# Optimization experiments

Measured on AMD Instinct MI355X. Metric: run time of the kernel, lower is better.

## Reference

```python
import jax, jax.numpy as jnp
import numpy as np

B_SZ, L, D_MODEL = 4, 4096, 512
D_INNER, N_HEADS, HEAD_DIM = 1024, 16, 64
D_STATE, D_CONV, CHUNK = 64, 4, 64
EPS = 1e-5


def setup_inputs() -> dict:
    key = jax.random.key(0)
    ks = jax.random.split(key, 12)
    return {
        'x': jax.random.normal(ks[0], (B_SZ, L, D_MODEL), jnp.float32),
        'W_in': jax.random.normal(ks[1], (D_MODEL, 2 * D_INNER), jnp.float32) * 0.02,
        'conv_x_kernel': jax.random.normal(ks[2], (D_CONV, 1, D_INNER), jnp.float32) * 0.1,
        'conv_x_bias': jnp.zeros((D_INNER,), jnp.float32),
        'conv_z_kernel': jax.random.normal(ks[3], (D_CONV, 1, D_INNER), jnp.float32) * 0.1,
        'conv_z_bias': jnp.zeros((D_INNER,), jnp.float32),
        'W_xdbl': jax.random.normal(ks[4], (D_INNER, N_HEADS + 2 * D_STATE), jnp.float32) * 0.02,
        'dt_bias': jax.random.normal(ks[5], (N_HEADS,), jnp.float32) * 0.5,
        'A_log': jax.random.uniform(ks[6], (N_HEADS,), jnp.float32, 0.0, 1.0),
        'D': jnp.ones((N_HEADS,), jnp.float32),
        'norm_weight': jnp.ones((D_INNER,), jnp.float32),
        'W_out': jax.random.normal(ks[7], (D_INNER, D_MODEL), jnp.float32) * 0.02,
    }


def dwconv(x, kernel, bias):
    # x: (b, l, d); kernel: (k, 1, d) depthwise, flax 'SAME' padding
    out = jax.lax.conv_general_dilated(
        x, kernel, window_strides=(1,), padding='SAME',
        dimension_numbers=('NWC', 'WIO', 'NWC'),
        feature_group_count=x.shape[-1])
    return out + bias


def segsum(a):
    # stable segment-sum: out[..., d, e] = sum_{e < i <= d} a[..., i]; -inf above diag
    T = a.shape[-1]
    a_rep = jnp.broadcast_to(a[..., :, None], a.shape + (T,))
    strict = jnp.tril(jnp.ones((T, T), bool), -1)
    seg = jnp.cumsum(jnp.where(strict, a_rep, 0.0), axis=-2)
    return jnp.where(jnp.tril(jnp.ones((T, T), bool)), seg, -jnp.inf)


def ssd(x, A, B, C, chunk):
    # x: (b,l,h,p), A: (b,l,h), B/C: (b,l,n) (single group, broadcast over heads)
    b, l, h, p = x.shape
    c = l // chunk
    x = x.reshape(b, c, chunk, h, p)
    A = A.reshape(b, c, chunk, h).transpose(0, 3, 1, 2)  # (b,h,c,l)
    B = B.reshape(b, c, chunk, -1)
    C = C.reshape(b, c, chunk, -1)
    A_cum = jnp.cumsum(A, axis=-1)
    Lmat = jnp.exp(segsum(A))  # (b,h,c,l,l)
    Y_diag = jnp.einsum('bcln,bcsn,bhcls,bcshp->bclhp', C, B, Lmat, x)
    decay_states = jnp.exp(A_cum[..., -1:] - A_cum)
    states = jnp.einsum('bcln,bhcl,bclhp->bchpn', B, decay_states, x)
    states = jnp.concatenate([jnp.zeros_like(states[:, :1]), states], axis=1)
    A_last = jnp.pad(A_cum[..., -1], ((0, 0), (0, 0), (1, 0)))
    decay_chunk = jnp.exp(segsum(A_last))  # (b,h,c+1,c+1)
    new_states = jnp.einsum('bhzc,bchpn->bzhpn', decay_chunk, states)
    states, final_state = new_states[:, :-1], new_states[:, -1]
    Y_off = jnp.einsum('bcln,bchpn,bhcl->bclhp', C, states, jnp.exp(A_cum))
    Y = (Y_diag + Y_off).reshape(b, l, h, p)
    return Y, final_state


def reference(x, W_in, conv_x_kernel, conv_x_bias, conv_z_kernel, conv_z_bias,
              W_xdbl, dt_bias, A_log, D, norm_weight, W_out):
    b, l, _ = x.shape
    xz = x @ W_in
    xi, z = jnp.split(xz, 2, axis=-1)
    xi = jax.nn.silu(dwconv(xi, conv_x_kernel, conv_x_bias))
    z = jax.nn.silu(dwconv(z, conv_z_kernel, conv_z_bias))
    x_dbl = xi @ W_xdbl  # (b,l,h+2n)
    dt = x_dbl[..., :N_HEADS]
    Bmat = x_dbl[..., N_HEADS:N_HEADS + D_STATE]
    Cmat = x_dbl[..., N_HEADS + D_STATE:]
    dt = jax.nn.softplus(dt + dt_bias)  # (b,l,h)
    A = -jnp.exp(A_log)  # (h,)
    xh = xi.reshape(b, l, N_HEADS, HEAD_DIM)
    y, _ = ssd(xh * dt[..., None], A * dt, Bmat, Cmat, CHUNK)
    y = y + xh * D[..., None]
    y = y.reshape(b, l, D_INNER)
    # gated RMSNorm (Mamba2 style): gate with silu(z), then rmsnorm with weight
    y = y * jax.nn.silu(z)
    y = y * jax.lax.rsqrt(jnp.mean(y * y, axis=-1, keepdims=True) + EPS) * norm_weight
    return y @ W_out
```

## Files before the change

### kernel.cpp

```cpp
#include <hip/hip_runtime.h>
#include <hip/hip_bf16.h>
#include <cstdint>

#define B_SZn 4
#define SEQ_L 4096
#define D_MODELn 512
#define D_INNERn 1024
#define N_HEADSn 16
#define HEAD_DIMn 64
#define D_STATEn 64
#define CHUNKn 64
#define NCHUNK (SEQ_L / CHUNKn)
#define BL (B_SZn * SEQ_L)
#define XDBL_N (N_HEADSn + 2 * D_STATEn)

typedef __hip_bfloat16 bf16;
typedef __bf16 bf16x8 __attribute__((ext_vector_type(8)));
typedef float f32x4 __attribute__((ext_vector_type(4)));

__device__ __forceinline__ float silu_f(float v) {
    return v / (1.0f + expf(-v));
}
__device__ __forceinline__ float b2f(unsigned short u) {
    return __uint_as_float((unsigned)u << 16);
}
__device__ __forceinline__ unsigned short f2b(float f) {
    bf16 h = __float2bfloat16(f);
    return *(unsigned short*)&h;
}
__device__ __forceinline__ void stf(float* p, float v) { *p = v; }
__device__ __forceinline__ void stf(bf16* p, float v) { *p = __float2bfloat16(v); }

__device__ __forceinline__ float4 us4_to_f4(ushort4 u) {
    float4 f;
    f.x = b2f(u.x); f.y = b2f(u.y); f.z = b2f(u.z); f.w = b2f(u.w);
    return f;
}

__device__ __forceinline__ void async_copy16(void* lds, const void* g) {
    __builtin_amdgcn_global_load_lds(
        (const __attribute__((address_space(1))) unsigned int*)g,
        (__attribute__((address_space(3))) unsigned int*)lds, 16, 0, 0);
}

__global__ __launch_bounds__(256) void cvt_f32_bf16(
    const float* __restrict__ in, bf16* __restrict__ out) {
    const int idx = blockIdx.x * 256 + threadIdx.x;
    float4 v = *(const float4*)(in + (size_t)idx * 4);
    ushort4 o;
    o.x = f2b(v.x); o.y = f2b(v.y); o.z = f2b(v.z); o.w = f2b(v.w);
    *(ushort4*)((unsigned short*)out + (size_t)idx * 4) = o;
}

__global__ __launch_bounds__(256) void transpose_cvt(
    const float* __restrict__ in, bf16* __restrict__ out, int R, int C) {
    __shared__ float t[32][33];
    const int bc = blockIdx.x * 32, br = blockIdx.y * 32;
    const int tx = threadIdx.x & 31, ty = threadIdx.x >> 5;
#pragma unroll
    for (int i = ty; i < 32; i += 8) {
        int r = br + i, c = bc + tx;
        t[i][tx] = (r < R && c < C) ? in[(size_t)r * C + c] : 0.f;
    }
    __syncthreads();
#pragma unroll
    for (int i = ty; i < 32; i += 8) {
        int c = bc + i, r = br + tx;
        if (c < C && r < R) out[(size_t)c * R + r] = __float2bfloat16(t[tx][i]);
    }
}

template <typename TO>
__global__ __launch_bounds__(256) void gemm_mfma(
    const bf16* __restrict__ A, const bf16* __restrict__ Bt,
    TO* __restrict__ C, int M, int N, int K) {
    __shared__ __align__(16) unsigned short Al[2][128 * 32];
    __shared__ __align__(16) unsigned short Bl[2][128 * 32];
    const int tid = threadIdx.x;
    const int wave = tid >> 6, lane = tid & 63;
    const int wm = (wave >> 1) * 64, wn = (wave & 1) * 64;
    int lin = blockIdx.y * gridDim.x + blockIdx.x;
    const int nwg = gridDim.x * gridDim.y;
    if ((nwg & 7) == 0) lin = (lin & 7) * (nwg >> 3) + (lin >> 3);
    const int bm = (lin / gridDim.x) * 128, bn = (lin % gridDim.x) * 128;
    f32x4 acc[4][4];
#pragma unroll
    for (int m = 0; m < 4; ++m)
#pragma unroll
        for (int n = 0; n < 4; ++n) acc[m][n] = (f32x4)(0.f);

    const int lrow = lane & 15, lk8 = (lane >> 4) * 8;
    const int srow = tid >> 2, sc8 = (tid & 3) * 8;
    for (int k0 = 0; k0 < K; k0 += 64) {
#pragma unroll
        for (int h = 0; h < 2; ++h) {
            const int kh = k0 + h * 32;
            async_copy16((char*)&Al[h][0] + (size_t)(wave * 64) * 16,
                         A + (size_t)(bm + srow) * K + kh + sc8);
            async_copy16((char*)&Al[h][0] + (size_t)(256 + wave * 64) * 16,
                         A + (size_t)(bm + 64 + srow) * K + kh + sc8);
            async_copy16((char*)&Bl[h][0] + (size_t)(wave * 64) * 16,
                         Bt + (size_t)(bn + srow) * K + kh + sc8);
            async_copy16((char*)&Bl[h][0] + (size_t)(256 + wave * 64) * 16,
                         Bt + (size_t)(bn + 64 + srow) * K + kh + sc8);
        }
        __syncthreads();
#pragma unroll
        for (int h = 0; h < 2; ++h) {
            bf16x8 af[4], bfr[4];
#pragma unroll
            for (int m = 0; m < 4; ++m)
                af[m] = *(const bf16x8*)(&Al[h][(wm + m * 16 + lrow) * 32 + lk8]);
#pragma unroll
            for (int n = 0; n < 4; ++n)
                bfr[n] = *(const bf16x8*)(&Bl[h][(wn + n * 16 + lrow) * 32 + lk8]);
#pragma unroll
            for (int m = 0; m < 4; ++m)
#pragma unroll
                for (int n = 0; n < 4; ++n)
                    acc[m][n] = __builtin_amdgcn_mfma_f32_16x16x32_bf16(
                        af[m], bfr[n], acc[m][n], 0, 0, 0);
        }
        __syncthreads();
    }
#pragma unroll
    for (int m = 0; m < 4; ++m) {
#pragma unroll
        for (int n = 0; n < 4; ++n) {
#pragma unroll
            for (int r = 0; r < 4; ++r) {
                int row = bm + wm + m * 16 + (lane >> 4) * 4 + r;
                int col = bn + wn + n * 16 + (lane & 15);
                if (row < M && col < N)
                    stf(&C[(size_t)row * N + col], acc[m][n][r]);
            }
        }
    }
}

template <typename TO>
__global__ __launch_bounds__(512) void gemm_mfma_wide(
    const bf16* __restrict__ A, const bf16* __restrict__ Bt,
    TO* __restrict__ C, int M, int N, int K) {
    __shared__ __align__(16) unsigned short Al[2][128 * 32];
    __shared__ __align__(16) unsigned short Bl[2][256 * 32];
    const int tid = threadIdx.x;
    const int wave = tid >> 6, lane = tid & 63;
    const int wm = (wave >> 2) * 64, wn = (wave & 3) * 64;
    int lin = blockIdx.y * gridDim.x + blockIdx.x;
    const int nwg = gridDim.x * gridDim.y;
    if ((nwg & 7) == 0) lin = (lin & 7) * (nwg >> 3) + (lin >> 3);
    const int bm = (lin / gridDim.x) * 128, bn = (lin % gridDim.x) * 256;
    f32x4 acc[4][4];
#pragma unroll
    for (int m = 0; m < 4; ++m)
#pragma unroll
        for (int n = 0; n < 4; ++n) acc[m][n] = (f32x4)(0.f);

    const int lrow = lane & 15, lk8 = (lane >> 4) * 8;
    const int srow = tid >> 2, sc8 = (tid & 3) * 8;
    for (int k0 = 0; k0 < K; k0 += 64) {
#pragma unroll
        for (int h = 0; h < 2; ++h) {
            const int kh = k0 + h * 32;
            async_copy16((char*)&Al[h][0] + (size_t)(wave * 64) * 16,
                         A + (size_t)(bm + srow) * K + kh + sc8);
            async_copy16((char*)&Bl[h][0] + (size_t)(wave * 64) * 16,
                         Bt + (size_t)(bn + srow) * K + kh + sc8);
            async_copy16((char*)&Bl[h][0] + (size_t)(512 + wave * 64) * 16,
                         Bt + (size_t)(bn + 128 + srow) * K + kh + sc8);
        }
        __syncthreads();
#pragma unroll
        for (int h = 0; h < 2; ++h) {
            bf16x8 af[4], bfr[4];
#pragma unroll
            for (int m = 0; m < 4; ++m)
                af[m] = *(const bf16x8*)(&Al[h][(wm + m * 16 + lrow) * 32 + lk8]);
#pragma unroll
            for (int n = 0; n < 4; ++n)
                bfr[n] = *(const bf16x8*)(&Bl[h][(wn + n * 16 + lrow) * 32 + lk8]);
#pragma unroll
            for (int m = 0; m < 4; ++m)
#pragma unroll
                for (int n = 0; n < 4; ++n)
                    acc[m][n] = __builtin_amdgcn_mfma_f32_16x16x32_bf16(
                        af[m], bfr[n], acc[m][n], 0, 0, 0);
        }
        __syncthreads();
    }
#pragma unroll
    for (int m = 0; m < 4; ++m) {
#pragma unroll
        for (int n = 0; n < 4; ++n) {
#pragma unroll
            for (int r = 0; r < 4; ++r) {
                int row = bm + wm + m * 16 + (lane >> 4) * 4 + r;
                int col = bn + wn + n * 16 + (lane & 15);
                if (row < M && col < N)
                    stf(&C[(size_t)row * N + col], acc[m][n][r]);
            }
        }
    }
}

__global__ __launch_bounds__(256) void conv_silu_kernel(
    const bf16* __restrict__ xz,
    const float* __restrict__ kx, const float* __restrict__ bx,
    const float* __restrict__ kz, const float* __restrict__ bz,
    bf16* __restrict__ xi, bf16* __restrict__ zo) {
    const int tid = threadIdx.x;
    const int d4 = tid * 4;
    const int blk = blockIdx.x;
    const int l0 = (blk * 8) & (SEQ_L - 1);
    const int b = (blk * 8) >> 12;
    const unsigned short* base = (const unsigned short*)xz +
                                 ((size_t)b * SEQ_L) * (2 * D_INNERn);
    float4 wx[4], wz[4];
#pragma unroll
    for (int k = 0; k < 4; ++k) {
        wx[k] = *(const float4*)(kx + k * D_INNERn + d4);
        wz[k] = *(const float4*)(kz + k * D_INNERn + d4);
    }
    const float4 bxv = *(const float4*)(bx + d4);
    const float4 bzv = *(const float4*)(bz + d4);
    float4 vx[4], vz[4];
#pragma unroll
    for (int j = 0; j < 3; ++j) {
        int l = l0 - 1 + j;
        if (l >= 0) {
            const unsigned short* row = base + (size_t)l * (2 * D_INNERn);
            vx[j] = us4_to_f4(*(const ushort4*)(row + d4));
            vz[j] = us4_to_f4(*(const ushort4*)(row + D_INNERn + d4));
        } else {
            vx[j] = make_float4(0.f, 0.f, 0.f, 0.f);
            vz[j] = make_float4(0.f, 0.f, 0.f, 0.f);
        }
    }
    unsigned short* xout = (unsigned short*)xi;
    unsigned short* zout = (unsigned short*)zo;
#pragma unroll
    for (int j = 0; j < 8; ++j) {
        const int lread = l0 + 2 + j;
        if (lread < SEQ_L) {
            const unsigned short* row = base + (size_t)lread * (2 * D_INNERn);
            vx[3] = us4_to_f4(*(const ushort4*)(row + d4));
            vz[3] = us4_to_f4(*(const ushort4*)(row + D_INNERn + d4));
        } else {
            vx[3] = make_float4(0.f, 0.f, 0.f, 0.f);
            vz[3] = make_float4(0.f, 0.f, 0.f, 0.f);
        }
        float4 ax = bxv, az = bzv;
#pragma unroll
        for (int k = 0; k < 4; ++k) {
            ax.x += vx[k].x * wx[k].x; ax.y += vx[k].y * wx[k].y;
            ax.z += vx[k].z * wx[k].z; ax.w += vx[k].w * wx[k].w;
            az.x += vz[k].x * wz[k].x; az.y += vz[k].y * wz[k].y;
            az.z += vz[k].z * wz[k].z; az.w += vz[k].w * wz[k].w;
        }
        ushort4 ox, oz;
        ox.x = f2b(silu_f(ax.x)); ox.y = f2b(silu_f(ax.y));
        ox.z = f2b(silu_f(ax.z)); ox.w = f2b(silu_f(ax.w));
        oz.x = f2b(silu_f(az.x)); oz.y = f2b(silu_f(az.y));
        oz.z = f2b(silu_f(az.z)); oz.w = f2b(silu_f(az.w));
        const size_t obase = ((size_t)b * SEQ_L + l0 + j) * D_INNERn + d4;
        *(ushort4*)(xout + obase) = ox;
        *(ushort4*)(zout + obase) = oz;
        vx[0] = vx[1]; vx[1] = vx[2]; vx[2] = vx[3];
        vz[0] = vz[1]; vz[1] = vz[2]; vz[2] = vz[3];
    }
}

__global__ __launch_bounds__(256) void ssd_chunk_mfma(
    const unsigned short* __restrict__ xdbl, const bf16* __restrict__ xi,
    const float* __restrict__ dt_bias, const float* __restrict__ A_log,
    const float* __restrict__ Dvec,
    unsigned short* __restrict__ y, unsigned short* __restrict__ S,
    float* __restrict__ acum_g, float* __restrict__ rchunk) {
    __shared__ __align__(16) unsigned short sBb[64 * 72];
    __shared__ __align__(16) unsigned short sCb[64 * 72];
    __shared__ __align__(16) unsigned short sXT[64 * 72];
    __shared__ __align__(16) unsigned short sGb[64 * 72];
    __shared__ __align__(16) unsigned short sWB[64 * 72];
    __shared__ float sdtp[64], sacum[64], sw[64];
    const int bid = blockIdx.x;
    const int h = bid & 15;
    const int bc = bid >> 4;
    const int c = bc & (NCHUNK - 1);
    const int b = bc >> 6;
    const int tid = threadIdx.x;
    const int wave = tid >> 6, lane = tid & 63;
    const int lrow = lane & 15, lk8 = (lane >> 4) * 8;
    const int row0 = b * SEQ_L + c * CHUNKn;
    const float Ah = -expf(A_log[h]);
    const float Dh = Dvec[h];

    if (tid < 64) {
        float v = b2f(xdbl[(size_t)(row0 + tid) * XDBL_N + h]) + dt_bias[h];
        sdtp[tid] = (v > 20.f) ? v : log1pf(expf(v));
    }
    const unsigned short* xius = (const unsigned short*)xi;
#pragma unroll
    for (int it = 0; it < 16; ++it) {
        int e = tid + it * 256;
        int s = e >> 6, n = e & 63;
        const unsigned short* xr = xdbl + (size_t)(row0 + s) * XDBL_N + N_HEADSn;
        sBb[s * 72 + n] = xr[n];
        sCb[s * 72 + n] = xr[D_STATEn + n];
        sXT[n * 72 + s] = xius[(size_t)(row0 + s) * D_INNERn + h * HEAD_DIMn + n];
    }
    __syncthreads();
    if (wave == 0) {
        float v = Ah * sdtp[lane];
#pragma unroll
        for (int o = 1; o < 64; o <<= 1) {
            float t = __shfl_up(v, o);
            if (lane >= o) v += t;
        }
        sacum[lane] = v;
        float last = __shfl(v, 63);
        sw[lane] = expf(last - v) * sdtp[lane];
        acum_g[(size_t)bid * 64 + lane] = v;
        if (lane == 63) rchunk[bid] = expf(v);
    }
    f32x4 acc1[4];
#pragma unroll
    for (int t = 0; t < 4; ++t) acc1[t] = (f32x4)(0.f);
    __builtin_amdgcn_s_setprio(1);
#pragma unroll
    for (int ks = 0; ks < 2; ++ks) {
        bf16x8 a = *(const bf16x8*)(&sCb[(wave * 16 + lrow) * 72 + ks * 32 + lk8]);
#pragma unroll
        for (int t = 0; t < 4; ++t) {
            bf16x8 bb = *(const bf16x8*)(&sBb[(t * 16 + lrow) * 72 + ks * 32 + lk8]);
            acc1[t] = __builtin_amdgcn_mfma_f32_16x16x32_bf16(a, bb, acc1[t], 0, 0, 0);
        }
    }
    __builtin_amdgcn_s_setprio(0);
    __syncthreads();
#pragma unroll
    for (int t = 0; t < 4; ++t) {
#pragma unroll
        for (int r = 0; r < 4; ++r) {
            int l = wave * 16 + (lane >> 4) * 4 + r;
            int s = t * 16 + lrow;
            float val = 0.f;
            if (l >= s) val = acc1[t][r] * expf(sacum[l] - sacum[s]) * sdtp[s];
            sGb[l * 72 + s] = f2b(val);
        }
    }
#pragma unroll
    for (int it = 0; it < 16; ++it) {
        int e = tid + it * 256;
        int s = e >> 6, n = e & 63;
        sWB[n * 72 + s] = f2b(sw[s] * b2f(sBb[s * 72 + n]));
    }
    __syncthreads();
    f32x4 acc2[4], acc3[4];
#pragma unroll
    for (int t = 0; t < 4; ++t) { acc2[t] = (f32x4)(0.f); acc3[t] = (f32x4)(0.f); }
    __builtin_amdgcn_s_setprio(1);
#pragma unroll
    for (int ks = 0; ks < 2; ++ks) {
        bf16x8 a2 = *(const bf16x8*)(&sGb[(wave * 16 + lrow) * 72 + ks * 32 + lk8]);
        bf16x8 a3 = *(const bf16x8*)(&sXT[(wave * 16 + lrow) * 72 + ks * 32 + lk8]);
#pragma unroll
        for (int t = 0; t < 4; ++t) {
            bf16x8 b2v = *(const bf16x8*)(&sXT[(t * 16 + lrow) * 72 + ks * 32 + lk8]);
            bf16x8 b3v = *(const bf16x8*)(&sWB[(t * 16 + lrow) * 72 + ks * 32 + lk8]);
            acc2[t] = __builtin_amdgcn_mfma_f32_16x16x32_bf16(a2, b2v, acc2[t], 0, 0, 0);
            acc3[t] = __builtin_amdgcn_mfma_f32_16x16x32_bf16(a3, b3v, acc3[t], 0, 0, 0);
        }
    }
    __builtin_amdgcn_s_setprio(0);
#pragma unroll
    for (int t = 0; t < 4; ++t) {
#pragma unroll
        for (int r = 0; r < 4; ++r) {
            int rr = wave * 16 + (lane >> 4) * 4 + r;
            int cc = t * 16 + lrow;
            float xv = b2f(sXT[cc * 72 + rr]);
            y[(size_t)(row0 + rr) * D_INNERn + h * HEAD_DIMn + cc] =
                f2b(acc2[t][r] + Dh * xv);
            S[(size_t)bid * 4096 + rr * 64 + cc] = f2b(acc3[t][r]);
        }
    }
}

__global__ __launch_bounds__(256) void chunk_scan_kernel(
    unsigned short* __restrict__ S, const float* __restrict__ rchunk) {
    const int idx = blockIdx.x * 256 + threadIdx.x;
    const int pn2 = (idx & 2047) * 2;
    const int bh = idx >> 11;
    const int h = bh & 15;
    const int b = bh >> 4;
    float P0 = 0.f, P1 = 0.f;
    for (int c = 0; c < NCHUNK; ++c) {
        int bid = (b * NCHUNK + c) * N_HEADSn + h;
        size_t off = (size_t)bid * 4096 + pn2;
        unsigned int v = *(unsigned int*)(S + off);
        float s0 = b2f((unsigned short)(v & 0xffff));
        float s1 = b2f((unsigned short)(v >> 16));
        *(unsigned int*)(S + off) =
            (unsigned int)f2b(P0) | ((unsigned int)f2b(P1) << 16);
        float rc = rchunk[bid];
        P0 = rc * P0 + s0;
        P1 = rc * P1 + s1;
    }
}

__global__ __launch_bounds__(256) void yoff_mfma(
    const unsigned short* __restrict__ xdbl, const unsigned short* __restrict__ S,
    const float* __restrict__ acum_g, unsigned short* __restrict__ y) {
    __shared__ __align__(16) unsigned short sCb[64 * 72];
    __shared__ __align__(16) unsigned short sP[64 * 72];
    __shared__ float se[64];
    const int bid = blockIdx.x;
    const int h = bid & 15;
    const int bc = bid >> 4;
    const int c = bc & (NCHUNK - 1);
    const int b = bc >> 6;
    const int tid = threadIdx.x;
    const int wave = tid >> 6, lane = tid & 63;
    const int lrow = lane & 15, lk8 = (lane >> 4) * 8;
    const int row0 = b * SEQ_L + c * CHUNKn;
    if (tid < 64) se[tid] = expf(acum_g[(size_t)bid * 64 + tid]);
#pragma unroll
    for (int it = 0; it < 16; ++it) {
        int e = tid + it * 256;
        int r = e >> 6, n = e & 63;
        sCb[r * 72 + n] = xdbl[(size_t)(row0 + r) * XDBL_N + N_HEADSn + D_STATEn + n];
        sP[r * 72 + n] = S[(size_t)bid * 4096 + e];
    }
    __syncthreads();
    f32x4 acc[4];
#pragma unroll
    for (int t = 0; t < 4; ++t) acc[t] = (f32x4)(0.f);
    __builtin_amdgcn_s_setprio(1);
#pragma unroll
    for (int ks = 0; ks < 2; ++ks) {
        bf16x8 a = *(const bf16x8*)(&sCb[(wave * 16 + lrow) * 72 + ks * 32 + lk8]);
#pragma unroll
        for (int t = 0; t < 4; ++t) {
            bf16x8 bb = *(const bf16x8*)(&sP[(t * 16 + lrow) * 72 + ks * 32 + lk8]);
            acc[t] = __builtin_amdgcn_mfma_f32_16x16x32_bf16(a, bb, acc[t], 0, 0, 0);
        }
    }
    __builtin_amdgcn_s_setprio(0);
#pragma unroll
    for (int t = 0; t < 4; ++t) {
#pragma unroll
        for (int r = 0; r < 4; ++r) {
            int l = wave * 16 + (lane >> 4) * 4 + r;
            int p = t * 16 + lrow;
            size_t idx = (size_t)(row0 + l) * D_INNERn + h * HEAD_DIMn + p;
            y[idx] = f2b(b2f(y[idx]) + acc[t][r] * se[l]);
        }
    }
}

__global__ __launch_bounds__(256) void gate_norm_kernel(
    const unsigned short* __restrict__ y, const bf16* __restrict__ zb,
    const float* __restrict__ nw, bf16* __restrict__ y_bf) {
    const int row = blockIdx.x;
    const int tid = threadIdx.x;
    const size_t base = (size_t)row * D_INNERn + tid * 4;
    ushort4 yu = *(const ushort4*)(y + base);
    ushort4 zu = *(const ushort4*)((const unsigned short*)zb + base);
    float v0 = b2f(yu.x) * silu_f(b2f(zu.x));
    float v1 = b2f(yu.y) * silu_f(b2f(zu.y));
    float v2 = b2f(yu.z) * silu_f(b2f(zu.z));
    float v3 = b2f(yu.w) * silu_f(b2f(zu.w));
    float ss = v0 * v0 + v1 * v1 + v2 * v2 + v3 * v3;
#pragma unroll
    for (int o = 32; o > 0; o >>= 1) ss += __shfl_xor(ss, o);
    __shared__ float sred[4];
    if ((tid & 63) == 0) sred[tid >> 6] = ss;
    __syncthreads();
    float total = sred[0] + sred[1] + sred[2] + sred[3];
    float scale = rsqrtf(total * (1.0f / D_INNERn) + 1e-5f);
    float4 wv = *(const float4*)(nw + tid * 4);
    ushort4 o4;
    o4.x = f2b(v0 * scale * wv.x);
    o4.y = f2b(v1 * scale * wv.y);
    o4.z = f2b(v2 * scale * wv.z);
    o4.w = f2b(v3 * scale * wv.w);
    *(ushort4*)((unsigned short*)y_bf + base) = o4;
}

extern "C" void kernel_launch(void* const* d_in, const int* in_sizes, int n_in,
                              void* d_out, int out_size, void* d_ws, size_t ws_size,
                              hipStream_t stream) {
    (void)in_sizes; (void)n_in; (void)out_size; (void)ws_size;
    const float* x       = (const float*)d_in[0];
    const float* W_in    = (const float*)d_in[1];
    const float* ckx     = (const float*)d_in[2];
    const float* cbx     = (const float*)d_in[3];
    const float* ckz     = (const float*)d_in[4];
    const float* cbz     = (const float*)d_in[5];
    const float* W_xdbl  = (const float*)d_in[6];
    const float* dt_bias = (const float*)d_in[7];
    const float* A_log   = (const float*)d_in[8];
    const float* Dvec    = (const float*)d_in[9];
    const float* nw      = (const float*)d_in[10];
    const float* W_out   = (const float*)d_in[11];
    float* out = (float*)d_out;
    char* w = (char*)d_ws;

    bf16*  xz     = (bf16*)(w);
    unsigned short* y = (unsigned short*)(w);
    bf16*  xi     = (bf16*)(w + 67108864);
    bf16*  zb     = (bf16*)(w + 100663296);
    char*  Sreg   = w + 134217728;
    unsigned short* S = (unsigned short*)Sreg;
    bf16*  x_bf   = (bf16*)Sreg;
    bf16*  W_in_T = (bf16*)(Sreg + 16777216);
    bf16*  W_xd_T = (bf16*)(Sreg + 18874368);
    bf16*  y_bf   = (bf16*)Sreg;
    bf16*  W_o_T  = (bf16*)(Sreg + 33554432);
    unsigned short* xdbl = (unsigned short*)(w + 201326592);
    float* acum   = (float*)(w + 211812352);
    float* rchunk = (float*)(w + 212860928);

    cvt_f32_bf16<<<BL * D_MODELn / 1024, 256, 0, stream>>>(x, x_bf);
    transpose_cvt<<<dim3(2048 / 32, 512 / 32), 256, 0, stream>>>(W_in, W_in_T, 512, 2048);
    transpose_cvt<<<dim3(5, 1024 / 32), 256, 0, stream>>>(W_xdbl, W_xd_T, 1024, 144);
    gemm_mfma_wide<bf16><<<dim3(2048 / 256, BL / 128), 512, 0, stream>>>(
        x_bf, W_in_T, xz, BL, 2048, D_MODELn);
    conv_silu_kernel<<<BL / 8, 256, 0, stream>>>(xz, ckx, cbx, ckz, cbz, xi, zb);
    gemm_mfma<bf16><<<dim3(2, BL / 128), 256, 0, stream>>>(
        xi, W_xd_T, (bf16*)xdbl, BL, XDBL_N, D_INNERn);
    ssd_chunk_mfma<<<B_SZn * NCHUNK * N_HEADSn, 256, 0, stream>>>(
        xdbl, xi, dt_bias, A_log, Dvec, y, S, acum, rchunk);
    chunk_scan_kernel<<<B_SZn * N_HEADSn * 2048 / 256, 256, 0, stream>>>(S, rchunk);
    yoff_mfma<<<B_SZn * NCHUNK * N_HEADSn, 256, 0, stream>>>(xdbl, S, acum, y);
    transpose_cvt<<<dim3(512 / 32, 1024 / 32), 256, 0, stream>>>(W_out, W_o_T, 1024, 512);
    gate_norm_kernel<<<BL, 256, 0, stream>>>(y, zb, nw, y_bf);
    gemm_mfma<float><<<dim3(512 / 128, BL / 128), 256, 0, stream>>>(
        y_bf, W_o_T, out, BL, D_MODELn, D_INNERn);
}
```

Before: 241.9 us.

## Software-pipeline GEMM K-loop with double-buffered async LDS loads

Both MFMA GEMM kernels now prefetch the next 32-wide K slice into the alternate LDS buffer while computing on the current one. Partial vmcnt waits let the previous stage's loads complete while the new ones stay in flight. Previously each 64-wide step loaded both halves, then computed, with no overlap between loads and MFMAs. The trade-off is twice as many barriers per unit of K and reliance on hand-set vmcnt counts matching the number of issued copies.

```diff
diff --git a/kernel.cpp b/kernel.cpp
--- a/kernel.cpp
+++ b/kernel.cpp
@@ -91,37 +91,43 @@
 
     const int lrow = lane & 15, lk8 = (lane >> 4) * 8;
     const int srow = tid >> 2, sc8 = (tid & 3) * 8;
-    for (int k0 = 0; k0 < K; k0 += 64) {
-#pragma unroll
-        for (int h = 0; h < 2; ++h) {
-            const int kh = k0 + h * 32;
-            async_copy16((char*)&Al[h][0] + (size_t)(wave * 64) * 16,
-                         A + (size_t)(bm + srow) * K + kh + sc8);
-            async_copy16((char*)&Al[h][0] + (size_t)(256 + wave * 64) * 16,
-                         A + (size_t)(bm + 64 + srow) * K + kh + sc8);
-            async_copy16((char*)&Bl[h][0] + (size_t)(wave * 64) * 16,
-                         Bt + (size_t)(bn + srow) * K + kh + sc8);
-            async_copy16((char*)&Bl[h][0] + (size_t)(256 + wave * 64) * 16,
-                         Bt + (size_t)(bn + 64 + srow) * K + kh + sc8);
-        }
-        __syncthreads();
-#pragma unroll
-        for (int h = 0; h < 2; ++h) {
-            bf16x8 af[4], bfr[4];
-#pragma unroll
-            for (int m = 0; m < 4; ++m)
-                af[m] = *(const bf16x8*)(&Al[h][(wm + m * 16 + lrow) * 32 + lk8]);
+    auto STAGE = [&](int buf, int k) {
+        async_copy16((char*)&Al[buf][0] + (size_t)(wave * 64) * 16,
+                     A + (size_t)(bm + srow) * K + k + sc8);
+        async_copy16((char*)&Al[buf][0] + (size_t)(256 + wave * 64) * 16,
+                     A + (size_t)(bm + 64 + srow) * K + k + sc8);
+        async_copy16((char*)&Bl[buf][0] + (size_t)(wave * 64) * 16,
+                     Bt + (size_t)(bn + srow) * K + k + sc8);
+        async_copy16((char*)&Bl[buf][0] + (size_t)(256 + wave * 64) * 16,
+                     Bt + (size_t)(bn + 64 + srow) * K + k + sc8);
+    };
+    STAGE(0, 0);
+    int cur = 0;
+    for (int k0 = 0; k0 < K; k0 += 32) {
+        if (k0 + 32 < K) {
+            STAGE(cur ^ 1, k0 + 32);
+            asm volatile("s_waitcnt vmcnt(4)" ::: "memory");
+        } else {
+            asm volatile("s_waitcnt vmcnt(0)" ::: "memory");
+        }
+        __builtin_amdgcn_sched_barrier(0);
+        __builtin_amdgcn_s_barrier();
+        bf16x8 af[4], bfr[4];
+#pragma unroll
+        for (int m = 0; m < 4; ++m)
+            af[m] = *(const bf16x8*)(&Al[cur][(wm + m * 16 + lrow) * 32 + lk8]);
+#pragma unroll
+        for (int n = 0; n < 4; ++n)
+            bfr[n] = *(const bf16x8*)(&Bl[cur][(wn + n * 16 + lrow) * 32 + lk8]);
+#pragma unroll
+        for (int m = 0; m < 4; ++m)
 #pragma unroll
             for (int n = 0; n < 4; ++n)
-                bfr[n] = *(const bf16x8*)(&Bl[h][(wn + n * 16 + lrow) * 32 + lk8]);
-#pragma unroll
-            for (int m = 0; m < 4; ++m)
-#pragma unroll
-                for (int n = 0; n < 4; ++n)
-                    acc[m][n] = __builtin_amdgcn_mfma_f32_16x16x32_bf16(
-                        af[m], bfr[n], acc[m][n], 0, 0, 0);
-        }
-        __syncthreads();
+                acc[m][n] = __builtin_amdgcn_mfma_f32_16x16x32_bf16(
+                    af[m], bfr[n], acc[m][n], 0, 0, 0);
+        __builtin_amdgcn_sched_barrier(0);
+        __builtin_amdgcn_s_barrier();
+        cur ^= 1;
     }
 #pragma unroll
     for (int m = 0; m < 4; ++m) {
@@ -159,35 +165,41 @@
 
     const int lrow = lane & 15, lk8 = (lane >> 4) * 8;
     const int srow = tid >> 2, sc8 = (tid & 3) * 8;
-    for (int k0 = 0; k0 < K; k0 += 64) {
-#pragma unroll
-        for (int h = 0; h < 2; ++h) {
-            const int kh = k0 + h * 32;
-            async_copy16((char*)&Al[h][0] + (size_t)(wave * 64) * 16,
-                         A + (size_t)(bm + srow) * K + kh + sc8);
-            async_copy16((char*)&Bl[h][0] + (size_t)(wave * 64) * 16,
-                         Bt + (size_t)(bn + srow) * K + kh + sc8);
-            async_copy16((char*)&Bl[h][0] + (size_t)(512 + wave * 64) * 16,
-                         Bt + (size_t)(bn + 128 + srow) * K + kh + sc8);
-        }
-        __syncthreads();
-#pragma unroll
-        for (int h = 0; h < 2; ++h) {
-            bf16x8 af[4], bfr[4];
-#pragma unroll
-            for (int m = 0; m < 4; ++m)
-                af[m] = *(const bf16x8*)(&Al[h][(wm + m * 16 + lrow) * 32 + lk8]);
+    auto STAGE = [&](int buf, int k) {
+        async_copy16((char*)&Al[buf][0] + (size_t)(wave * 64) * 16,
+                     A + (size_t)(bm + srow) * K + k + sc8);
+        async_copy16((char*)&Bl[buf][0] + (size_t)(wave * 64) * 16,
+                     Bt + (size_t)(bn + srow) * K + k + sc8);
+        async_copy16((char*)&Bl[buf][0] + (size_t)(512 + wave * 64) * 16,
+                     Bt + (size_t)(bn + 128 + srow) * K + k + sc8);
+    };
+    STAGE(0, 0);
+    int cur = 0;
+    for (int k0 = 0; k0 < K; k0 += 32) {
+        if (k0 + 32 < K) {
+            STAGE(cur ^ 1, k0 + 32);
+            asm volatile("s_waitcnt vmcnt(3)" ::: "memory");
+        } else {
+            asm volatile("s_waitcnt vmcnt(0)" ::: "memory");
+        }
+        __builtin_amdgcn_sched_barrier(0);
+        __builtin_amdgcn_s_barrier();
+        bf16x8 af[4], bfr[4];
+#pragma unroll
+        for (int m = 0; m < 4; ++m)
+            af[m] = *(const bf16x8*)(&Al[cur][(wm + m * 16 + lrow) * 32 + lk8]);
+#pragma unroll
+        for (int n = 0; n < 4; ++n)
+            bfr[n] = *(const bf16x8*)(&Bl[cur][(wn + n * 16 + lrow) * 32 + lk8]);
+#pragma unroll
+        for (int m = 0; m < 4; ++m)
 #pragma unroll
             for (int n = 0; n < 4; ++n)
-                bfr[n] = *(const bf16x8*)(&Bl[h][(wn + n * 16 + lrow) * 32 + lk8]);
-#pragma unroll
-            for (int m = 0; m < 4; ++m)
-#pragma unroll
-                for (int n = 0; n < 4; ++n)
-                    acc[m][n] = __builtin_amdgcn_mfma_f32_16x16x32_bf16(
-                        af[m], bfr[n], acc[m][n], 0, 0, 0);
-        }
-        __syncthreads();
+                acc[m][n] = __builtin_amdgcn_mfma_f32_16x16x32_bf16(
+                    af[m], bfr[n], acc[m][n], 0, 0, 0);
+        __builtin_amdgcn_sched_barrier(0);
+        __builtin_amdgcn_s_barrier();
+        cur ^= 1;
     }
 #pragma unroll
     for (int m = 0; m < 4; ++m) {
```

Result: no change. 245.4 us (+1.4%).
